# Optimization experiments

Hardware: AMD Instinct MI355X
Metric: run time of the kernel (lower is better)

Reference implementation:

```python
import jax, jax.numpy as jnp
import numpy as np

VOCAB = 30000
EMB = 100
HID = 300
SEQ = 200
BATCH = 4096


def setup_inputs() -> dict:
    key = jax.random.key(0)
    ks = jax.random.split(key, 10)
    s_ih = 1.0 / np.sqrt(HID)
    inp = {
        "x": jax.random.randint(ks[0], (SEQ, BATCH), 0, VOCAB, dtype=jnp.int64) if jax.config.jax_enable_x64 else jax.random.randint(ks[0], (SEQ, BATCH), 0, VOCAB, dtype=jnp.int32),
        "emb": jax.random.normal(ks[1], (VOCAB, EMB), dtype=jnp.float32),
        "w_ih": jax.random.uniform(ks[2], (HID, EMB), jnp.float32, -s_ih, s_ih),
        "w_hh": jax.random.uniform(ks[3], (HID, HID), jnp.float32, -s_ih, s_ih),
        "b_ih": jax.random.uniform(ks[4], (HID,), jnp.float32, -s_ih, s_ih),
        "b_hh": jax.random.uniform(ks[5], (HID,), jnp.float32, -s_ih, s_ih),
        "fc1_w": jax.random.uniform(ks[6], (256, HID), jnp.float32, -1/np.sqrt(HID), 1/np.sqrt(HID)),
        "fc1_b": jax.random.uniform(ks[7], (256,), jnp.float32, -1/np.sqrt(HID), 1/np.sqrt(HID)),
        "fc2_w": jax.random.uniform(ks[8], (3, 256), jnp.float32, -1/np.sqrt(256), 1/np.sqrt(256)),
        "fc2_b": jax.random.uniform(ks[9], (3,), jnp.float32, -1/np.sqrt(256), 1/np.sqrt(256)),
    }
    return inp


def reference(x, emb, w_ih, w_hh, b_ih, b_hh, fc1_w, fc1_b, fc2_w, fc2_b):
    # Embedding lookup: [SEQ, BATCH] -> [SEQ, BATCH, EMB]
    xe = emb[x]
    # Precompute input projections for all timesteps (same math, more efficient)
    xp = jnp.einsum('sbe,he->sbh', xe, w_ih) + b_ih + b_hh  # [SEQ, BATCH, HID]
    h0 = jnp.zeros((x.shape[1], HID), dtype=emb.dtype)

    def step(h, xt):
        h = jnp.tanh(xt + h @ w_hh.T)
        return h, None

    ht, _ = jax.lax.scan(step, h0, xp)
    h1 = jax.nn.relu(ht @ fc1_w.T + fc1_b)
    out = h1 @ fc2_w.T + fc2_b
    return out
```

## Files before the change

### kernel.cpp

```cpp
#include <hip/hip_runtime.h>


#define SEQ    200
#define BATCHN 4096
#define EMBD   100
#define HIDN   300

#define KCH   10
#define KCE   4
#define XE0   320
#define BSPAN 448
#define SROW  904
#define ROWS  16

typedef _Float16 half8 __attribute__((ext_vector_type(8)));
typedef float    f32x4 __attribute__((ext_vector_type(4)));

static __device__ __forceinline__ f32x4 f4z() { f32x4 z = {0.f, 0.f, 0.f, 0.f}; return z; }

static __device__ __forceinline__ half8 h8cvt(f32x4 a, f32x4 b) {
  half8 h;
  h[0]=(_Float16)a[0]; h[1]=(_Float16)a[1]; h[2]=(_Float16)a[2]; h[3]=(_Float16)a[3];
  h[4]=(_Float16)b[0]; h[5]=(_Float16)b[1]; h[6]=(_Float16)b[2]; h[7]=(_Float16)b[3];
  return h;
}

static __device__ __forceinline__ half8 loadw(const float* row, int k0, int kmax, bool nv) {
  f32x4 a = (nv && (k0 + 3 < kmax)) ? *(const f32x4*)(row + k0)     : f4z();
  f32x4 b = (nv && (k0 + 7 < kmax)) ? *(const f32x4*)(row + k0 + 4) : f4z();
  return h8cvt(a, b);
}

static __device__ __forceinline__ float tanh_fast(float x) {
  float e = __builtin_amdgcn_exp2f(x * 2.8853900817779268f);
  float r = __builtin_amdgcn_rcpf(e + 1.0f);
  return __builtin_fmaf(-2.0f, r, 1.0f);
}

#define MFMA32(A,B,C) __builtin_amdgcn_mfma_f32_16x16x32_f16((A),(B),(C),0,0,0)

#define STEP_BODY(NT_) do {                                                   \
    _Pragma("unroll")                                                         \
    for (int c = 0; c < KCH; c++) {                                           \
      const half8 a = *(const half8*)(ab + c * 32);                           \
      acc[0] = MFMA32(a, whh[c][0], acc[0]);                                  \
      acc[1] = MFMA32(a, whh[c][1], acc[1]);                                  \
      if (NT_ == 3) acc[2] = MFMA32(a, whh[c][2], acc[2]);                    \
    }                                                                         \
    _Pragma("unroll")                                                         \
    for (int c = 0; c < KCE; c++) {                                           \
      const half8 a = *(const half8*)(ab + XE0 + c * 32);                     \
      acc[0] = MFMA32(a, wih[c][0], acc[0]);                                  \
      acc[1] = MFMA32(a, wih[c][1], acc[1]);                                  \
      if (NT_ == 3) acc[2] = MFMA32(a, wih[c][2], acc[2]);                    \
    }                                                                         \
  } while (0)

__global__ __launch_bounds__(512, 2)
void rnn_fused(const int* __restrict__ x, const float* __restrict__ emb,
               const float* __restrict__ w_ih, const float* __restrict__ w_hh,
               const float* __restrict__ b_ih, const float* __restrict__ b_hh,
               const float* __restrict__ fc1w, const float* __restrict__ fc1b,
               const float* __restrict__ fc2w, const float* __restrict__ fc2b,
               float* __restrict__ out)
{
  __shared__ __align__(16) _Float16 s_lds[ROWS][SROW];
  __shared__ __align__(16) float    h1f[ROWS][257];
  __shared__ int x_lds[SEQ][16];

  const int tid  = (int)threadIdx.x;
  const int lane = tid & 63;
  const int wv   = tid >> 6;
  const int r    = lane & 15;
  const int g    = lane >> 4;
  const int base = (int)blockIdx.x * ROWS;

  const int t0    = (wv < 3) ? wv * 3 : 9 + (wv - 3) * 2;
  const int ntile = (wv < 3) ? 3 : 2;

  for (int i = tid; i < SEQ * 16; i += 512)
    x_lds[i >> 4][i & 15] = x[(i >> 4) * BATCHN + base + (i & 15)];
  for (int i = tid; i < ROWS * SROW; i += 512)
    (&s_lds[0][0])[i] = (_Float16)0.f;

  half8 whh[KCH][3];
  half8 wih[KCE][3];
  float bias[3];
  #pragma unroll
  for (int tt = 0; tt < 3; tt++) {
    const int n = (t0 + tt) * 16 + r;
    const bool nv = (tt < ntile) && (n < HIDN);
    bias[tt] = nv ? (b_ih[n] + b_hh[n]) : 0.f;
    #pragma unroll
    for (int c = 0; c < KCH; c++)
      whh[c][tt] = loadw(w_hh + (long)n * HIDN, c * 32 + 8 * g, HIDN, nv);
    #pragma unroll
    for (int c = 0; c < KCE; c++)
      wih[c][tt] = loadw(w_ih + (long)n * EMBD, c * 32 + 8 * g, EMBD, nv);
  }

  const int gc0 = (wv - 6) * 2;

  __syncthreads();

  if (wv >= 6) {
    const int idx = x_lds[0][r];
    const float* erow = emb + (long)idx * EMBD;
    #pragma unroll
    for (int j = 0; j < 2; j++) {
      const int k0 = (gc0 + j) * 32 + 8 * g;
      f32x4 a = (k0 + 3 < EMBD) ? *(const f32x4*)(erow + k0)     : f4z();
      f32x4 b = (k0 + 7 < EMBD) ? *(const f32x4*)(erow + k0 + 4) : f4z();
      *(half8*)&s_lds[r][XE0 + k0] = h8cvt(a, b);
    }
  }
  __syncthreads();

  const _Float16* a_base = &s_lds[r][8 * g];

  #pragma unroll 2
  for (int t = 0; t < SEQ; t++) {
    const _Float16* ab = a_base + (t & 1) * BSPAN;
    const int nbuf = ((t + 1) & 1) * BSPAN;

    f32x4 xg[2][2];
    if (wv >= 6) {
      const int tn = (t + 1 < SEQ) ? t + 1 : t;
      const int idx = x_lds[tn][r];
      const float* erow = emb + (long)idx * EMBD;
      #pragma unroll
      for (int j = 0; j < 2; j++) {
        const int k0 = (gc0 + j) * 32 + 8 * g;
        xg[j][0] = (k0 + 3 < EMBD) ? *(const f32x4*)(erow + k0)     : f4z();
        xg[j][1] = (k0 + 7 < EMBD) ? *(const f32x4*)(erow + k0 + 4) : f4z();
      }
    }

    f32x4 acc[3];
    #pragma unroll
    for (int tt = 0; tt < 3; tt++) {
      f32x4 v = {bias[tt], bias[tt], bias[tt], bias[tt]};
      acc[tt] = v;
    }

    if (ntile == 3) { STEP_BODY(3); } else { STEP_BODY(2); }

    if (wv >= 6) {
      #pragma unroll
      for (int j = 0; j < 2; j++) {
        const int k0 = (gc0 + j) * 32 + 8 * g;
        *(half8*)&s_lds[r][nbuf + XE0 + k0] = h8cvt(xg[j][0], xg[j][1]);
      }
    }
    #pragma unroll
    for (int tt = 0; tt < 3; tt++) {
      if (tt < ntile) {
        const int n = (t0 + tt) * 16 + r;
        if (n < HIDN) {
          #pragma unroll
          for (int j = 0; j < 4; j++)
            s_lds[4 * g + j][nbuf + n] = (_Float16)tanh_fast(acc[tt][j]);
        }
      }
    }
    __syncthreads();
  }

  {
    const _Float16* abf = a_base + (SEQ & 1) * BSPAN;
    f32x4 acc1[2];
    const int f0 = wv * 2;
    #pragma unroll
    for (int ft = 0; ft < 2; ft++) {
      const float bb = fc1b[(f0 + ft) * 16 + r];
      f32x4 v = {bb, bb, bb, bb};
      acc1[ft] = v;
    }
    #pragma unroll
    for (int c = 0; c < KCH; c++) {
      const half8 a = *(const half8*)(abf + c * 32);
      #pragma unroll
      for (int ft = 0; ft < 2; ft++) {
        const int n = (f0 + ft) * 16 + r;
        const half8 b = loadw(fc1w + (long)n * HIDN, c * 32 + 8 * g, HIDN, true);
        acc1[ft] = MFMA32(a, b, acc1[ft]);
      }
    }
    #pragma unroll
    for (int ft = 0; ft < 2; ft++) {
      const int n = (f0 + ft) * 16 + r;
      #pragma unroll
      for (int j = 0; j < 4; j++) {
        const float v = acc1[ft][j];
        h1f[4 * g + j][n] = v > 0.f ? v : 0.f;
      }
    }
  }
  __syncthreads();

  if (wv == 0 && lane < 48) {
    const int m = lane / 3;
    const int n = lane - 3 * m;
    float s = fc2b[n];
    for (int k = 0; k < 256; k++)
      s = __builtin_fmaf(h1f[m][k], fc2w[n * 256 + k], s);
    out[(base + m) * 3 + n] = s;
  }
}

extern "C" void kernel_launch(void* const* d_in, const int* in_sizes, int n_in,
                              void* d_out, int out_size, void* d_ws, size_t ws_size,
                              hipStream_t stream) {
  (void)in_sizes; (void)n_in; (void)d_ws; (void)ws_size; (void)out_size;
  const int*   x   = (const int*)d_in[0];
  const float* emb = (const float*)d_in[1];
  const float* wih = (const float*)d_in[2];
  const float* whh = (const float*)d_in[3];
  const float* bih = (const float*)d_in[4];
  const float* bhh = (const float*)d_in[5];
  const float* f1w = (const float*)d_in[6];
  const float* f1b = (const float*)d_in[7];
  const float* f2w = (const float*)d_in[8];
  const float* f2b = (const float*)d_in[9];
  rnn_fused<<<BATCHN / ROWS, 512, 0, stream>>>(
      x, emb, wih, whh, bih, bhh, f1w, f1b, f2w, f2b, (float*)d_out);
}
```

Measured before the change: 337.6 us.

## Halve block to 4 waves with 5 tiles each, add XOR-swizzled LDS layout

Each block now runs 4 wavefronts of 256 threads instead of 8, so each wave owns up to 5 output tiles of 16 hidden units. Per-wave weights held in registers grow, and each A fragment read from LDS feeds more MFMAs. The hidden-state and embedding buffers are addressed in bytes with an XOR swizzle on the row index to cut LDS bank conflicts. All waves now share the embedding gather, which previously fell only to two waves. The cost is higher register pressure, since whh/wih grow to 70 half8 per thread, and fewer waves available to hide per-step latency and barrier stalls.

```diff
diff --git a/kernel.cpp b/kernel.cpp
--- a/kernel.cpp
+++ b/kernel.cpp
@@ -8,15 +8,16 @@
 
 #define KCH   10
 #define KCE   4
-#define XE0   320
-#define BSPAN 448
-#define SROW  904
+#define XE0B  640
+#define BUFB  896
+#define SROWB 1792
 #define ROWS  16
+#define NTMAX 5
 
 typedef _Float16 half8 __attribute__((ext_vector_type(8)));
 typedef float    f32x4 __attribute__((ext_vector_type(4)));
 
-static __device__ __forceinline__ f32x4 f4z() { f32x4 z = {0.f, 0.f, 0.f, 0.f}; return z; }
+static __device__ __forceinline__ f32x4 f4z() { f32x4 z = {0.f,0.f,0.f,0.f}; return z; }
 
 static __device__ __forceinline__ half8 h8cvt(f32x4 a, f32x4 b) {
   half8 h;
@@ -39,24 +40,30 @@
 
 #define MFMA32(A,B,C) __builtin_amdgcn_mfma_f32_16x16x32_f16((A),(B),(C),0,0,0)
 
+#define AREAD(boff) (*(const half8*)(lds_base + ((boff) ^ swz)))
+
 #define STEP_BODY(NT_) do {                                                   \
     _Pragma("unroll")                                                         \
     for (int c = 0; c < KCH; c++) {                                           \
-      const half8 a = *(const half8*)(ab + c * 32);                           \
+      const half8 a = AREAD(rbuf + c * 64 + g16);                             \
       acc[0] = MFMA32(a, whh[c][0], acc[0]);                                  \
       acc[1] = MFMA32(a, whh[c][1], acc[1]);                                  \
-      if (NT_ == 3) acc[2] = MFMA32(a, whh[c][2], acc[2]);                    \
+      acc[2] = MFMA32(a, whh[c][2], acc[2]);                                  \
+      acc[3] = MFMA32(a, whh[c][3], acc[3]);                                  \
+      if (NT_ == 5) acc[4] = MFMA32(a, whh[c][4], acc[4]);                    \
     }                                                                         \
     _Pragma("unroll")                                                         \
     for (int c = 0; c < KCE; c++) {                                           \
-      const half8 a = *(const half8*)(ab + XE0 + c * 32);                     \
+      const half8 a = AREAD(rbuf + XE0B + c * 64 + g16);                      \
       acc[0] = MFMA32(a, wih[c][0], acc[0]);                                  \
       acc[1] = MFMA32(a, wih[c][1], acc[1]);                                  \
-      if (NT_ == 3) acc[2] = MFMA32(a, wih[c][2], acc[2]);                    \
+      acc[2] = MFMA32(a, wih[c][2], acc[2]);                                  \
+      acc[3] = MFMA32(a, wih[c][3], acc[3]);                                  \
+      if (NT_ == 5) acc[4] = MFMA32(a, wih[c][4], acc[4]);                    \
     }                                                                         \
   } while (0)
 
-__global__ __launch_bounds__(512, 2)
+__global__ __launch_bounds__(256, 1)
 void rnn_fused(const int* __restrict__ x, const float* __restrict__ emb,
                const float* __restrict__ w_ih, const float* __restrict__ w_hh,
                const float* __restrict__ b_ih, const float* __restrict__ b_hh,
@@ -64,8 +71,8 @@
                const float* __restrict__ fc2w, const float* __restrict__ fc2b,
                float* __restrict__ out)
 {
-  __shared__ __align__(16) _Float16 s_lds[ROWS][SROW];
-  __shared__ __align__(16) float    h1f[ROWS][257];
+  __shared__ __align__(128) char s_lds[ROWS * SROWB];
+  __shared__ __align__(16) float h1f[ROWS][257];
   __shared__ int x_lds[SEQ][16];
 
   const int tid  = (int)threadIdx.x;
@@ -73,21 +80,23 @@
   const int wv   = tid >> 6;
   const int r    = lane & 15;
   const int g    = lane >> 4;
+  const int g16  = 16 * g;
   const int base = (int)blockIdx.x * ROWS;
-
-  const int t0    = (wv < 3) ? wv * 3 : 9 + (wv - 3) * 2;
-  const int ntile = (wv < 3) ? 3 : 2;
-
-  for (int i = tid; i < SEQ * 16; i += 512)
+  const int swz  = (r & 7) << 4;
+
+  const int t0    = wv * NTMAX;
+  const int ntile = (wv < 3) ? 5 : 4;
+
+  for (int i = tid; i < SEQ * 16; i += 256)
     x_lds[i >> 4][i & 15] = x[(i >> 4) * BATCHN + base + (i & 15)];
-  for (int i = tid; i < ROWS * SROW; i += 512)
-    (&s_lds[0][0])[i] = (_Float16)0.f;
-
-  half8 whh[KCH][3];
-  half8 wih[KCE][3];
-  float bias[3];
+  for (int i = tid; i < ROWS * SROWB / 4; i += 256)
+    ((int*)s_lds)[i] = 0;
+
+  half8 whh[KCH][NTMAX];
+  half8 wih[KCE][NTMAX];
+  float bias[NTMAX];
   #pragma unroll
-  for (int tt = 0; tt < 3; tt++) {
+  for (int tt = 0; tt < NTMAX; tt++) {
     const int n = (t0 + tt) * 16 + r;
     const bool nv = (tt < ntile) && (n < HIDN);
     bias[tt] = nv ? (b_ih[n] + b_hh[n]) : 0.f;
@@ -99,67 +108,56 @@
       wih[c][tt] = loadw(w_ih + (long)n * EMBD, c * 32 + 8 * g, EMBD, nv);
   }
 
-  const int gc0 = (wv - 6) * 2;
+  const int rr = r;
+  const int sl = wv * 4 + g;
+  const int k0 = 8 * sl;
+  char* const lds_base = s_lds + r * SROWB;
+  char* const xw_base  = s_lds + rr * SROWB;
 
   __syncthreads();
 
-  if (wv >= 6) {
-    const int idx = x_lds[0][r];
+  {
+    const int idx = x_lds[0][rr];
     const float* erow = emb + (long)idx * EMBD;
-    #pragma unroll
-    for (int j = 0; j < 2; j++) {
-      const int k0 = (gc0 + j) * 32 + 8 * g;
-      f32x4 a = (k0 + 3 < EMBD) ? *(const f32x4*)(erow + k0)     : f4z();
-      f32x4 b = (k0 + 7 < EMBD) ? *(const f32x4*)(erow + k0 + 4) : f4z();
-      *(half8*)&s_lds[r][XE0 + k0] = h8cvt(a, b);
-    }
+    f32x4 a = (k0 + 3 < EMBD) ? *(const f32x4*)(erow + k0)     : f4z();
+    f32x4 b = (k0 + 7 < EMBD) ? *(const f32x4*)(erow + k0 + 4) : f4z();
+    *(half8*)(xw_base + ((XE0B + 16 * sl) ^ ((rr & 7) << 4))) = h8cvt(a, b);
   }
   __syncthreads();
-
-  const _Float16* a_base = &s_lds[r][8 * g];
 
   #pragma unroll 2
   for (int t = 0; t < SEQ; t++) {
-    const _Float16* ab = a_base + (t & 1) * BSPAN;
-    const int nbuf = ((t + 1) & 1) * BSPAN;
-
-    f32x4 xg[2][2];
-    if (wv >= 6) {
-      const int tn = (t + 1 < SEQ) ? t + 1 : t;
-      const int idx = x_lds[tn][r];
-      const float* erow = emb + (long)idx * EMBD;
-      #pragma unroll
-      for (int j = 0; j < 2; j++) {
-        const int k0 = (gc0 + j) * 32 + 8 * g;
-        xg[j][0] = (k0 + 3 < EMBD) ? *(const f32x4*)(erow + k0)     : f4z();
-        xg[j][1] = (k0 + 7 < EMBD) ? *(const f32x4*)(erow + k0 + 4) : f4z();
-      }
-    }
-
-    f32x4 acc[3];
-    #pragma unroll
-    for (int tt = 0; tt < 3; tt++) {
+    const int rbuf = (t & 1) * BUFB;
+    const int wbuf = ((t + 1) & 1) * BUFB;
+
+    const int tn = (t + 1 < SEQ) ? t + 1 : t;
+    const int idx = x_lds[tn][rr];
+    const float* erow = emb + (long)idx * EMBD;
+    f32x4 xga = (k0 + 3 < EMBD) ? *(const f32x4*)(erow + k0)     : f4z();
+    f32x4 xgb = (k0 + 7 < EMBD) ? *(const f32x4*)(erow + k0 + 4) : f4z();
+
+    f32x4 acc[NTMAX];
+    #pragma unroll
+    for (int tt = 0; tt < NTMAX; tt++) {
       f32x4 v = {bias[tt], bias[tt], bias[tt], bias[tt]};
       acc[tt] = v;
     }
 
-    if (ntile == 3) { STEP_BODY(3); } else { STEP_BODY(2); }
-
-    if (wv >= 6) {
-      #pragma unroll
-      for (int j = 0; j < 2; j++) {
-        const int k0 = (gc0 + j) * 32 + 8 * g;
-        *(half8*)&s_lds[r][nbuf + XE0 + k0] = h8cvt(xg[j][0], xg[j][1]);
-      }
-    }
-    #pragma unroll
-    for (int tt = 0; tt < 3; tt++) {
+    if (ntile == 5) { STEP_BODY(5); } else { STEP_BODY(4); }
+
+    *(half8*)(xw_base + ((wbuf + XE0B + 16 * sl) ^ ((rr & 7) << 4))) = h8cvt(xga, xgb);
+
+    #pragma unroll
+    for (int tt = 0; tt < NTMAX; tt++) {
       if (tt < ntile) {
         const int n = (t0 + tt) * 16 + r;
         if (n < HIDN) {
           #pragma unroll
-          for (int j = 0; j < 4; j++)
-            s_lds[4 * g + j][nbuf + n] = (_Float16)tanh_fast(acc[tt][j]);
+          for (int j = 0; j < 4; j++) {
+            const int m = 4 * g + j;
+            *(_Float16*)(s_lds + m * SROWB + ((wbuf + 2 * n) ^ ((m & 7) << 4)))
+                = (_Float16)tanh_fast(acc[tt][j]);
+          }
         }
       }
     }
@@ -167,27 +165,27 @@
   }
 
   {
-    const _Float16* abf = a_base + (SEQ & 1) * BSPAN;
-    f32x4 acc1[2];
-    const int f0 = wv * 2;
-    #pragma unroll
-    for (int ft = 0; ft < 2; ft++) {
+    const int fbuf = (SEQ & 1) * BUFB;
+    f32x4 acc1[4];
+    const int f0 = wv * 4;
+    #pragma unroll
+    for (int ft = 0; ft < 4; ft++) {
       const float bb = fc1b[(f0 + ft) * 16 + r];
       f32x4 v = {bb, bb, bb, bb};
       acc1[ft] = v;
     }
     #pragma unroll
     for (int c = 0; c < KCH; c++) {
-      const half8 a = *(const half8*)(abf + c * 32);
+      const half8 a = AREAD(fbuf + c * 64 + g16);
       #pragma unroll
-      for (int ft = 0; ft < 2; ft++) {
+      for (int ft = 0; ft < 4; ft++) {
         const int n = (f0 + ft) * 16 + r;
         const half8 b = loadw(fc1w + (long)n * HIDN, c * 32 + 8 * g, HIDN, true);
         acc1[ft] = MFMA32(a, b, acc1[ft]);
       }
     }
     #pragma unroll
-    for (int ft = 0; ft < 2; ft++) {
+    for (int ft = 0; ft < 4; ft++) {
       const int n = (f0 + ft) * 16 + r;
       #pragma unroll
       for (int j = 0; j < 4; j++) {
@@ -222,6 +220,6 @@
   const float* f1b = (const float*)d_in[7];
   const float* f2w = (const float*)d_in[8];
   const float* f2b = (const float*)d_in[9];
-  rnn_fused<<<BATCHN / ROWS, 512, 0, stream>>>(
+  rnn_fused<<<BATCHN / ROWS, 256, 0, stream>>>(
       x, emb, wih, whh, bih, bhh, f1w, f1b, f2w, f2b, (float*)d_out);
 }
```

After: 451.7 us. +33.8%, slower.
